# Kernel tuning notes

Measured on AMD Instinct MI355X. Metric: run time of the kernel, lower is better.

Reference implementation:

```python
import jax, jax.numpy as jnp
import numpy as np

HEADS = 8
DIM_HEAD = 64
NUM_PATHWAYS = 281
SCALE = DIM_HEAD ** -0.5


def setup_inputs() -> dict:
    key = jax.random.key(0)
    k1, k2 = jax.random.split(key)
    b, n, dim = 4, 12281, 512  # n = 281 pathway tokens + 12000 histology patch tokens
    x = jax.random.normal(k1, (b, n, dim), dtype=jnp.float32)
    W_qkv = jax.random.normal(k2, (dim, 3 * HEADS * DIM_HEAD), dtype=jnp.float32) * 0.02
    return {"x": x, "W_qkv": W_qkv}


def reference(x, W_qkv):
    b, n, _ = x.shape
    h, d, m = HEADS, DIM_HEAD, NUM_PATHWAYS
    qkv = x @ W_qkv  # [b, n, 3*h*d]
    q, k, v = jnp.split(qkv, 3, axis=-1)
    # [b, n, h*d] -> [b, h, n, d]
    to_bhnd = lambda t: t.reshape(b, n, h, d).transpose(0, 2, 1, 3)
    q, k, v = to_bhnd(q), to_bhnd(k), to_bhnd(v)
    q = q * SCALE

    q_path, q_hist = q[:, :, :m], q[:, :, m:]
    k_path, k_hist = k[:, :, :m], k[:, :, m:]
    v_path, v_hist = v[:, :, :m], v[:, :, m:]

    # histology queries attend to pathway keys: [b, h, n_hist, m]
    attn_hist = jax.nn.softmax(jnp.einsum('bhid,bhjd->bhij', q_hist, k_path), axis=-1)
    # pathway queries attend to histology keys: [b, h, m, n_hist]
    attn_path = jax.nn.softmax(jnp.einsum('bhid,bhjd->bhij', q_path, k_hist), axis=-1)

    out_pathways = jnp.einsum('bhij,bhjd->bhid', attn_hist, v_path)   # [b, h, n_hist, d]
    out_histology = jnp.einsum('bhij,bhjd->bhid', attn_path, v_hist)  # [b, h, m, d]

    cross_token = jnp.concatenate([out_pathways, out_histology], axis=2)  # [b, h, n, d]
    return cross_token.transpose(0, 2, 1, 3).reshape(b, n, h * d)
```

## Files before the change

### kernel.cpp

```cpp
#include <hip/hip_runtime.h>
#include <hip/hip_bf16.h>

#define BATCH  4
#define NTOK   12281
#define DIMIN  512
#define HEADS  8
#define DHEAD  64
#define MPATH  281
#define NHIST  12000
#define QKVC   1536
#define QSCALE 0.180336884f
#define ROWS   (BATCH * NTOK)
#define MPAD   49152
#define NSPLIT 16
#define KSPL   768
#define PROWS  320
#define HROWS  12032
#define M1B    640
#define M0B    1504
#define QPAD   4096

typedef __attribute__((ext_vector_type(8)))  short        short8v;
typedef __attribute__((ext_vector_type(4)))  float        f32x4;
typedef __attribute__((ext_vector_type(16))) float        f32x16;
typedef __attribute__((ext_vector_type(4)))  unsigned int uint4v;

__device__ __forceinline__ unsigned short f2bf(float f) {
    unsigned x = __builtin_bit_cast(unsigned, f);
    return (unsigned short)((x + 0x7fffu + ((x >> 16) & 1u)) >> 16);
}
__device__ __forceinline__ unsigned pk2(float a, float b) {
    return (unsigned)f2bf(a) | ((unsigned)f2bf(b) << 16);
}
__device__ __forceinline__ unsigned pk2n(float a, float b) {
    unsigned r;
    asm("v_cvt_pk_bf16_f32 %0, %1, %2" : "=v"(r) : "v"(a), "v"(b));
    return r;
}
__device__ __forceinline__ void plswap(unsigned &a, unsigned &b) {
    asm("v_permlane32_swap_b32 %0, %1" : "+v"(a), "+v"(b));
}
__device__ __forceinline__ float fexp2(float x) {
    return __builtin_amdgcn_exp2f(x);
}
__device__ __forceinline__ short8v ld8(const unsigned short* p) {
    return *reinterpret_cast<const short8v*>(p);
}
__device__ __forceinline__ f32x16 MFMA32(short8v a, short8v b, f32x16 c) {
    return __builtin_amdgcn_mfma_f32_32x32x16_bf16(a, b, c, 0, 0, 0);
}
__device__ __forceinline__ void gl16(const char* g, char* l) {
    __builtin_amdgcn_global_load_lds(
        (const __attribute__((address_space(1))) unsigned int*)g,
        (__attribute__((address_space(3))) unsigned int*)l, 16, 0, 0);
}

__global__ __launch_bounds__(256)
void convert_x(const float* __restrict__ x, unsigned short* __restrict__ xb)
{
    size_t i = ((size_t)blockIdx.x * 256 + threadIdx.x) * 8;
    if (i >= (size_t)MPAD * DIMIN) return;
    uint4v o;
    if (i < (size_t)ROWS * DIMIN) {
        float4 a = *reinterpret_cast<const float4*>(x + i);
        float4 b = *reinterpret_cast<const float4*>(x + i + 4);
        o[0] = pk2(a.x, a.y); o[1] = pk2(a.z, a.w);
        o[2] = pk2(b.x, b.y); o[3] = pk2(b.z, b.w);
    } else {
        o[0] = o[1] = o[2] = o[3] = 0u;
    }
    *reinterpret_cast<uint4v*>(xb + i) = o;
}

__global__ __launch_bounds__(256)
void wt_convert(const float* __restrict__ w, unsigned short* __restrict__ wt)
{
    __shared__ unsigned short Ls[64][72];
    const int k0 = blockIdx.x * 64;
    const int n0 = blockIdx.y * 64;
    const int t  = threadIdx.x;
    const int lr = t >> 2;
    const int c0 = (t & 3) * 16;

    const float* sp = w + (size_t)(k0 + lr) * QKVC + n0 + c0;
    #pragma unroll
    for (int j = 0; j < 16; j += 4) {
        float4 a = *reinterpret_cast<const float4*>(sp + j);
        Ls[lr][c0 + j + 0] = f2bf(a.x);
        Ls[lr][c0 + j + 1] = f2bf(a.y);
        Ls[lr][c0 + j + 2] = f2bf(a.z);
        Ls[lr][c0 + j + 3] = f2bf(a.w);
    }
    __syncthreads();

    alignas(16) unsigned short tmp[16];
    #pragma unroll
    for (int j = 0; j < 16; ++j) tmp[j] = Ls[c0 + j][lr];
    unsigned short* dp = wt + (size_t)(n0 + lr) * DIMIN + k0 + c0;
    *reinterpret_cast<short8v*>(dp)     = *reinterpret_cast<short8v*>(&tmp[0]);
    *reinterpret_cast<short8v*>(dp + 8) = *reinterpret_cast<short8v*>(&tmp[8]);
}

__global__ __launch_bounds__(256)
void pad_fill(unsigned short* kpth, unsigned short* vpth,
              unsigned short* khst, unsigned short* vhst)
{
    int i = blockIdx.x * 256 + threadIdx.x;
    const int PPAD = (PROWS - MPATH) * DHEAD;
    const int HPAD = (HROWS - NHIST) * DHEAD;
    if (i < 32 * PPAD) {
        int bh = i / PPAD, r = i - bh * PPAD;
        size_t off = ((size_t)bh * PROWS + MPATH) * DHEAD + r;
        kpth[off] = 0; vpth[off] = 0;
    }
    if (i < 32 * HPAD) {
        int bh = i / HPAD, r = i - bh * HPAD;
        size_t off = ((size_t)bh * HROWS + NHIST) * DHEAD + r;
        khst[off] = 0; vhst[off] = 0;
    }
}

__global__ __launch_bounds__(256, 2)
void qkv_mfma(const unsigned short* __restrict__ xb, const unsigned short* __restrict__ wt,
              unsigned short* __restrict__ qb,
              unsigned short* __restrict__ kpth, unsigned short* __restrict__ khst,
              unsigned short* __restrict__ vpth, unsigned short* __restrict__ vhst)
{
    __shared__ char lds[65536];
    const int tid  = threadIdx.x;
    const int lane = tid & 63;
    const int wid  = tid >> 6;
    const int wr   = wid >> 1;
    const int wc   = wid & 1;

    int id  = blockIdx.x;
    int wg  = (id & 7) * 576 + (id >> 3);
    const int mt = wg / 12, nt = wg - mt * 12;
    const int bm = mt * 128, bn = nt * 128;

    const int arow0 = tid >> 3;
    const int acolS = ((tid & 7) << 4) ^ ((arow0 & 7) << 4);
    const char* xsrc = (const char*)xb + (((size_t)(bm + arow0)) << 10) + acolS;
    const char* wsrc = (const char*)wt + (((size_t)(bn + arow0)) << 10) + acolS;
    char* ldsA = lds + wid * 1024;
    char* ldsB = lds + 16384 + wid * 1024;

    const int rA   = wr * 64 + (lane & 15);
    const int rB   = wc * 64 + (lane & 15);
    const int hi16 = (lane >> 4) << 4;
    const int sxA  = (rA & 7) << 4;
    const int sxB  = (rB & 7) << 4;

    f32x4 acc[4][4];
    #pragma unroll
    for (int m = 0; m < 4; ++m)
        #pragma unroll
        for (int n = 0; n < 4; ++n)
            #pragma unroll
            for (int r = 0; r < 4; ++r) acc[m][n][r] = 0.f;

    auto STAGE = [&](int bufofs, int ks) {
        const char* xs = xsrc + (size_t)ks * 128;
        const char* ws = wsrc + (size_t)ks * 128;
        #pragma unroll
        for (int i = 0; i < 4; ++i)
            gl16(xs + ((size_t)i << 15), ldsA + bufofs + i * 4096);
        #pragma unroll
        for (int i = 0; i < 4; ++i)
            gl16(ws + ((size_t)i << 15), ldsB + bufofs + i * 4096);
    };

    STAGE(0, 0);
    asm volatile("s_waitcnt vmcnt(0)" ::: "memory");
    __syncthreads();

    for (int ks = 0; ks < 8; ++ks) {
        const int cur = ks & 1;
        if (ks < 7) STAGE((cur ^ 1) * 32768, ks + 1);

        const char* A = lds + cur * 32768;
        const char* B = A + 16384;
        #pragma unroll
        for (int kk = 0; kk < 2; ++kk) {
            short8v a[4], b[4];
            #pragma unroll
            for (int m = 0; m < 4; ++m)
                a[m] = *reinterpret_cast<const short8v*>(
                    A + (rA + m * 16) * 128 + ((kk * 64 + hi16) ^ sxA));
            #pragma unroll
            for (int n = 0; n < 4; ++n)
                b[n] = *reinterpret_cast<const short8v*>(
                    B + (rB + n * 16) * 128 + ((kk * 64 + hi16) ^ sxB));
            #pragma unroll
            for (int m = 0; m < 4; ++m)
                #pragma unroll
                for (int n = 0; n < 4; ++n)
                    acc[m][n] = __builtin_amdgcn_mfma_f32_16x16x32_bf16(
                        a[m], b[n], acc[m][n], 0, 0, 0);
        }
        asm volatile("s_waitcnt vmcnt(0)" ::: "memory");
        __syncthreads();
    }

    unsigned short* cl = reinterpret_cast<unsigned short*>(lds);
    const int crow0 = (lane >> 4) * 4;
    const int ccol  = lane & 15;
    #pragma unroll
    for (int n = 0; n < 4; ++n) {
        const int gcb = bn + wc * 64 + n * 16;
        const float scl = (gcb < 512) ? QSCALE : 1.f;
        #pragma unroll
        for (int m = 0; m < 4; ++m) {
            #pragma unroll
            for (int r = 0; r < 4; ++r) {
                int row = wr * 64 + m * 16 + crow0 + r;
                int col = wc * 64 + n * 16 + ccol;
                cl[row * 136 + col] = f2bf(acc[m][n][r] * scl);
            }
        }
    }
    __syncthreads();

    #pragma unroll
    for (int i = 0; i < 8; ++i) {
        const int chunk = tid + i * 256;
        const int row = chunk >> 4;
        const int c8  = (chunk & 15) * 8;
        const int grow = bm + row;
        if (grow < ROWS) {
            uint4v val = *reinterpret_cast<const uint4v*>(cl + row * 136 + c8);
            const int gcol  = bn + c8;
            const int which = gcol >> 9;
            const int rem   = gcol & 511;
            const int hh = rem >> 6, dd = rem & 63;
            const int bb = grow / NTOK;
            const int nn = grow - bb * NTOK;
            const int bh = bb * HEADS + hh;
            unsigned short* dst;
            if (which == 0) {
                dst = qb + ((size_t)bh * NTOK + nn) * DHEAD + dd;
            } else if (which == 1) {
                dst = (nn < MPATH) ? kpth + ((size_t)bh * PROWS + nn) * DHEAD + dd
                                   : khst + ((size_t)bh * HROWS + (nn - MPATH)) * DHEAD + dd;
            } else {
                dst = (nn < MPATH) ? vpth + ((size_t)bh * PROWS + nn) * DHEAD + dd
                                   : vhst + ((size_t)bh * HROWS + (nn - MPATH)) * DHEAD + dd;
            }
            *reinterpret_cast<uint4v*>(dst) = val;
        }
    }
}

__global__ __launch_bounds__(256)
void transpose64(const unsigned short* __restrict__ src, unsigned short* __restrict__ dst,
                 int nrpad)
{
    __shared__ unsigned short Ls[64][72];
    const int bh = blockIdx.y;
    const int r0 = blockIdx.x * 64;
    const unsigned short* s = src + (size_t)bh * nrpad * DHEAD;
    unsigned short*       d = dst + (size_t)bh * nrpad * DHEAD;

    const int t  = threadIdx.x;
    const int lr = t >> 2;
    const int c0 = (t & 3) * 16;

    const unsigned short* sp = s + (size_t)(r0 + lr) * DHEAD + c0;
    *reinterpret_cast<short8v*>(&Ls[lr][c0])     = *reinterpret_cast<const short8v*>(sp);
    *reinterpret_cast<short8v*>(&Ls[lr][c0 + 8]) = *reinterpret_cast<const short8v*>(sp + 8);
    __syncthreads();

    alignas(16) unsigned short tmp[16];
    #pragma unroll
    for (int j = 0; j < 16; ++j) tmp[j] = Ls[c0 + j][lr];
    const int T  = (r0 + c0) >> 5;
    const int kk = (r0 + c0) & 31;
    unsigned short* dp = d + (((size_t)T * 64 + lr) << 5) + kk;
    *reinterpret_cast<short8v*>(dp)     = *reinterpret_cast<short8v*>(&tmp[0]);
    *reinterpret_cast<short8v*>(dp + 8) = *reinterpret_cast<short8v*>(&tmp[8]);
}

#define ATTN_BODY(VC0,VC1,VC2,VC3,VN0,VN1,VN2,VN3,TT)                      \
  do {                                                                     \
    __builtin_amdgcn_s_setprio(1);                                         \
    f32x16 sA = MFMA32(kf0, qA0, SZ);                                      \
    sA = MFMA32(kf1, qA1, sA);                                             \
    sA = MFMA32(kf2, qA2, sA);                                             \
    sA = MFMA32(kf3, qA3, sA);                                             \
    f32x16 sB = MFMA32(kf0, qB0, SZ);                                      \
    sB = MFMA32(kf1, qB1, sB);                                             \
    sB = MFMA32(kf2, qB2, sB);                                             \
    sB = MFMA32(kf3, qB3, sB);                                             \
    __builtin_amdgcn_s_setprio(0);                                         \
    if ((TT) + 1 < ntiles) {               \
      const unsigned short* kn = kr + (size_t)((TT) + 1) * 2048;           \
      kf0 = ld8(kn);      kf1 = ld8(kn + 16);                              \
      kf2 = ld8(kn + 32); kf3 = ld8(kn + 48);                              \
      const unsigned short* vn = vb + (size_t)((TT) + 1) * 2048;           \
      VN0 = ld8(vn);        VN1 = ld8(vn + 16);                            \
      VN2 = ld8(vn + 1024); VN3 = ld8(vn + 1040);                          \
    }                                                                      \
    float psA = 0.f, psB = 0.f;                                            \
    if (mode0 && (TT) == 8) {                   \
      _Pragma("unroll")                                                    \
      for (int r = 0; r < 16; ++r) {                                       \
        int krow = (r & 3) + 8 * (r >> 2) + 4 * hi;                        \
        float eA = (256 + krow >= MPATH) ? 0.f : fexp2(sA[r]);             \
        float eB = (256 + krow >= MPATH) ? 0.f : fexp2(sB[r]);             \
        sA[r] = eA; psA += eA;                                             \
        sB[r] = eB; psB += eB;                                             \
      }                                                                    \
    } else {                                                               \
      _Pragma("unroll")                                                    \
      for (int r = 0; r < 16; ++r) {                                       \
        float eA = fexp2(sA[r]); sA[r] = eA; psA += eA;                    \
        float eB = fexp2(sB[r]); sB[r] = eB; psB += eB;                    \
      }                                                                    \
    }                                                                      \
    lA += psA; lB += psB;                                                  \
    unsigned A0 = pk2n(sA[0],  sA[1]),  A1 = pk2n(sA[2],  sA[3]);          \
    unsigned A2 = pk2n(sA[4],  sA[5]),  A3 = pk2n(sA[6],  sA[7]);          \
    unsigned A4 = pk2n(sA[8],  sA[9]),  A5 = pk2n(sA[10], sA[11]);         \
    unsigned A6 = pk2n(sA[12], sA[13]), A7 = pk2n(sA[14], sA[15]);         \
    plswap(A0, A2); plswap(A1, A3); plswap(A4, A6); plswap(A5, A7);        \
    uint4v wA0, wA1;                                                       \
    wA0[0] = A0; wA0[1] = A1; wA0[2] = A2; wA0[3] = A3;                    \
    wA1[0] = A4; wA1[1] = A5; wA1[2] = A6; wA1[3] = A7;                    \
    short8v paA0 = __builtin_bit_cast(short8v, wA0);                       \
    short8v paA1 = __builtin_bit_cast(short8v, wA1);                       \
    unsigned B0 = pk2n(sB[0],  sB[1]),  B1 = pk2n(sB[2],  sB[3]);          \
    unsigned B2 = pk2n(sB[4],  sB[5]),  B3 = pk2n(sB[6],  sB[7]);          \
    unsigned B4 = pk2n(sB[8],  sB[9]),  B5 = pk2n(sB[10], sB[11]);         \
    unsigned B6 = pk2n(sB[12], sB[13]), B7 = pk2n(sB[14], sB[15]);         \
    plswap(B0, B2); plswap(B1, B3); plswap(B4, B6); plswap(B5, B7);        \
    uint4v wB0, wB1;                                                       \
    wB0[0] = B0; wB0[1] = B1; wB0[2] = B2; wB0[3] = B3;                    \
    wB1[0] = B4; wB1[1] = B5; wB1[2] = B6; wB1[3] = B7;                    \
    short8v paB0 = __builtin_bit_cast(short8v, wB0);                       \
    short8v paB1 = __builtin_bit_cast(short8v, wB1);                       \
    __builtin_amdgcn_s_setprio(1);                                         \
    o0 = MFMA32(paA0, VC0, o0);                                            \
    o0 = MFMA32(paA1, VC1, o0);                                            \
    o1 = MFMA32(paA0, VC2, o1);                                            \
    o1 = MFMA32(paA1, VC3, o1);                                            \
    o2 = MFMA32(paB0, VC0, o2);                                            \
    o2 = MFMA32(paB1, VC1, o2);                                            \
    o3 = MFMA32(paB0, VC2, o3);                                            \
    o3 = MFMA32(paB1, VC3, o3);                                            \
    __builtin_amdgcn_s_setprio(0);                                         \
  } while (0)

__global__ __launch_bounds__(256, 2)
void fused_attn(const unsigned short* __restrict__ qbuf,
                const unsigned short* __restrict__ kpth, const unsigned short* __restrict__ khst,
                const unsigned short* __restrict__ vtp,  const unsigned short* __restrict__ vth,
                float* __restrict__ out,
                float* __restrict__ pl, float* __restrict__ po)
{
    const int wave = threadIdx.x >> 6;
    const int lane = threadIdx.x & 63;
    const int hi   = lane >> 5;
    const int ql   = lane & 31;

    int bh, pw, sp = 0;
    bool mode0;
    if (blockIdx.x < M1B) {
        mode0 = false;
        const int xcd = blockIdx.x & 7;
        const int j   = blockIdx.x >> 3;
        const int w   = j * 4 + wave;
        const int spi = w / 160;
        const int rem = w - spi * 160;
        bh = rem / 5;
        pw = rem - bh * 5;
        sp = xcd + 8 * spi;
    } else {
        mode0 = true;
        const int b0  = blockIdx.x - M1B;
        const int xcd = b0 & 7;
        const int i   = b0 >> 3;
        const int g   = i / 47;
        bh = xcd + 8 * g;
        pw = (i - g * 47) * 4 + wave;
    }

    const int q0 = mode0 ? (MPATH + pw * 64) : (pw * 64);
    const unsigned short* qra = qbuf + ((size_t)bh * NTOK + (q0 + ql)) * DHEAD + hi * 8;
    const unsigned short* qrb = qra + (size_t)32 * DHEAD;
    short8v qA0 = ld8(qra),      qA1 = ld8(qra + 16);
    short8v qA2 = ld8(qra + 32), qA3 = ld8(qra + 48);
    short8v qB0 = ld8(qrb),      qB1 = ld8(qrb + 16);
    short8v qB2 = ld8(qrb + 32), qB3 = ld8(qrb + 48);

    const unsigned short* kr;
    const unsigned short* vb;
    int ntiles;
    if (mode0) {
        kr = kpth + (size_t)bh * PROWS * DHEAD + ql * DHEAD + hi * 8;
        vb = vtp  + (size_t)bh * PROWS * DHEAD + ql * 32 + hi * 8;
        ntiles = 9;
    } else {
        kr = khst + ((size_t)bh * HROWS + (size_t)sp * KSPL) * DHEAD + ql * DHEAD + hi * 8;
        vb = vth  + (size_t)bh * HROWS * DHEAD + (size_t)sp * 24 * 2048 + ql * 32 + hi * 8;
        ntiles = (sp == NSPLIT - 1) ? 15 : 24;
    }

    f32x16 o0, o1, o2, o3, SZ;
    #pragma unroll
    for (int r = 0; r < 16; ++r) { o0[r] = 0.f; o1[r] = 0.f; o2[r] = 0.f; o3[r] = 0.f; SZ[r] = 0.f; }
    float lA = 0.f, lB = 0.f;

    short8v kf0 = ld8(kr), kf1 = ld8(kr + 16), kf2 = ld8(kr + 32), kf3 = ld8(kr + 48);
    short8v va0 = ld8(vb),        va1 = ld8(vb + 16);
    short8v va2 = ld8(vb + 1024), va3 = ld8(vb + 1040);
    short8v vb0 = va0, vb1 = va1, vb2 = va2, vb3 = va3;

    for (int t = 0;;) {
        ATTN_BODY(va0, va1, va2, va3, vb0, vb1, vb2, vb3, t);
        if (++t >= ntiles) break;
        ATTN_BODY(vb0, vb1, vb2, vb3, va0, va1, va2, va3, t);
        if (++t >= ntiles) break;
    }

    const float lAr = lA + __shfl_xor(lA, 32);
    const float lBr = lB + __shfl_xor(lB, 32);

    if (mode0) {
        const int bb = bh >> 3, hh = bh & 7;
        const float liA = 1.0f / lAr;
        const float liB = 1.0f / lBr;
        #pragma unroll
        for (int r = 0; r < 16; ++r) {
            const int row = (r & 3) + 8 * (r >> 2) + 4 * hi;
            {
                float invr = __shfl(liA, row);
                float* op = out + ((size_t)bb * NTOK + (pw * 64 + row)) * (HEADS * DHEAD) + hh * DHEAD;
                op[ql]      = o0[r] * invr;
                op[32 + ql] = o1[r] * invr;
            }
            const int tokB = pw * 64 + 32 + row;
            if (tokB < NHIST) {
                float invr = __shfl(liB, row);
                float* op = out + ((size_t)bb * NTOK + tokB) * (HEADS * DHEAD) + hh * DHEAD;
                op[ql]      = o2[r] * invr;
                op[32 + ql] = o3[r] * invr;
            }
        }
    } else {
        const size_t pbase = ((size_t)bh * NSPLIT + sp) * MPATH;
        if (hi == 0) {
            if (q0 + ql < MPATH)      pl[pbase + q0 + ql]      = lAr;
            if (q0 + 32 + ql < MPATH) pl[pbase + q0 + 32 + ql] = lBr;
        }
        #pragma unroll
        for (int r = 0; r < 16; ++r) {
            const int row = (r & 3) + 8 * (r >> 2) + 4 * hi;
            const int qqA = q0 + row;
            if (qqA < MPATH) {
                float* pp = po + (pbase + qqA) * DHEAD;
                pp[ql]      = o0[r];
                pp[32 + ql] = o1[r];
            }
            const int qqB = q0 + 32 + row;
            if (qqB < MPATH) {
                float* pp = po + (pbase + qqB) * DHEAD;
                pp[ql]      = o2[r];
                pp[32 + ql] = o3[r];
            }
        }
    }
}

__global__ __launch_bounds__(256)
void combine_kernel(const float* __restrict__ pl, const float* __restrict__ po,
                    float* __restrict__ out)
{
    const int idx = blockIdx.x * 256 + threadIdx.x;
    const int dd  = idx & 63;
    const int r   = idx >> 6;
    if (r >= BATCH * HEADS * MPATH) return;
    const int bh = r / MPATH;
    const int jq = r - bh * MPATH;

    const size_t pbase = ((size_t)bh * NSPLIT) * MPATH + jq;
    float L = 0.f, acc = 0.f;
    #pragma unroll
    for (int s = 0; s < NSPLIT; ++s) {
        L   += pl[pbase + (size_t)s * MPATH];
        acc += po[(pbase + (size_t)s * MPATH) * DHEAD + dd];
    }
    const int bb = bh >> 3, hh = bh & 7;
    out[((size_t)bb * NTOK + (NHIST + jq)) * (HEADS * DHEAD) + hh * DHEAD + dd] = acc / L;
}

extern "C" void kernel_launch(void* const* d_in, const int* in_sizes, int n_in,
                              void* d_out, int out_size, void* d_ws, size_t ws_size,
                              hipStream_t stream)
{
    (void)in_sizes; (void)n_in; (void)out_size; (void)ws_size;
    const float* x = (const float*)d_in[0];
    const float* w = (const float*)d_in[1];
    float* out = (float*)d_out;

    const size_t QEL = (size_t)32 * NTOK * DHEAD + QPAD;
    const size_t PEL = (size_t)32 * PROWS * DHEAD;
    const size_t HEL = (size_t)32 * HROWS * DHEAD;

    unsigned short* qb   = (unsigned short*)d_ws;
    unsigned short* kpth = qb   + QEL;
    unsigned short* khst = kpth + PEL;
    unsigned short* vpth = khst + HEL;
    unsigned short* vhst = vpth + PEL;
    unsigned short* vtp  = vhst + HEL;
    unsigned short* vth  = vtp  + PEL;
    unsigned short* xb   = vth  + HEL;
    unsigned short* wtb  = xb   + (size_t)MPAD * DIMIN;
    float* pl = (float*)(wtb + (size_t)QKVC * DIMIN);
    float* po = pl + (size_t)32 * NSPLIT * MPATH;

    convert_x<<<(MPAD * DIMIN / 8 + 255) / 256, 256, 0, stream>>>(x, xb);
    wt_convert<<<dim3(DIMIN / 64, QKVC / 64), 256, 0, stream>>>(w, wtb);
    pad_fill<<<312, 256, 0, stream>>>(kpth, vpth, khst, vhst);

    qkv_mfma<<<(MPAD / 128) * (QKVC / 128), 256, 0, stream>>>(xb, wtb, qb,
                                                              kpth, khst, vpth, vhst);

    transpose64<<<dim3(PROWS / 64, 32), 256, 0, stream>>>(vpth, vtp, PROWS);
    transpose64<<<dim3(HROWS / 64, 32), 256, 0, stream>>>(vhst, vth, HROWS);

    fused_attn<<<M1B + M0B, 256, 0, stream>>>(qb, kpth, khst, vtp, vth, out, pl, po);

    const int rows = BATCH * HEADS * MPATH;
    combine_kernel<<<(rows * DHEAD + 255) / 256, 256, 0, stream>>>(pl, po, out);
}
```

Measured before the change: 282.2 us.

## Merge prep kernels into one launch and compute softmax row sums via MFMA

The three preprocessing kernels (x conversion, weight transpose/convert, pad zeroing) are merged into one launch that dispatches on block index, removing two kernel launches and their gaps. In the attention kernel, the per-tile scalar accumulation of exponentiated scores is replaced by extra MFMAs against a vector of bf16 ones, which yields row sums already laid out per output row. This removes the cross-lane shuffles and scalar adds, at the cost of four extra MFMAs per tile, two more 16-register accumulators, and sums computed from bf16-rounded probabilities, which changes precision slightly. The final division now uses a raw hardware reciprocal instruction.

```diff
diff --git a/kernel.cpp b/kernel.cpp
--- a/kernel.cpp
+++ b/kernel.cpp
@@ -19,6 +19,9 @@
 #define M1B    640
 #define M0B    1504
 #define QPAD   4096
+#define NB_CONV 12288
+#define NB_WT   192
+#define NB_PAD  312
 
 typedef __attribute__((ext_vector_type(8)))  short        short8v;
 typedef __attribute__((ext_vector_type(4)))  float        f32x4;
@@ -43,6 +46,11 @@
 __device__ __forceinline__ float fexp2(float x) {
     return __builtin_amdgcn_exp2f(x);
 }
+__device__ __forceinline__ float frcp(float x) {
+    float r;
+    asm("v_rcp_f32 %0, %1" : "=v"(r) : "v"(x));
+    return r;
+}
 __device__ __forceinline__ short8v ld8(const unsigned short* p) {
     return *reinterpret_cast<const short8v*>(p);
 }
@@ -56,67 +64,65 @@
 }
 
 __global__ __launch_bounds__(256)
-void convert_x(const float* __restrict__ x, unsigned short* __restrict__ xb)
-{
-    size_t i = ((size_t)blockIdx.x * 256 + threadIdx.x) * 8;
-    if (i >= (size_t)MPAD * DIMIN) return;
-    uint4v o;
-    if (i < (size_t)ROWS * DIMIN) {
-        float4 a = *reinterpret_cast<const float4*>(x + i);
-        float4 b = *reinterpret_cast<const float4*>(x + i + 4);
-        o[0] = pk2(a.x, a.y); o[1] = pk2(a.z, a.w);
-        o[2] = pk2(b.x, b.y); o[3] = pk2(b.z, b.w);
-    } else {
-        o[0] = o[1] = o[2] = o[3] = 0u;
-    }
-    *reinterpret_cast<uint4v*>(xb + i) = o;
-}
-
-__global__ __launch_bounds__(256)
-void wt_convert(const float* __restrict__ w, unsigned short* __restrict__ wt)
+void prep_all(const float* __restrict__ x, unsigned short* __restrict__ xb,
+              const float* __restrict__ w, unsigned short* __restrict__ wt,
+              unsigned short* kpth, unsigned short* vpth,
+              unsigned short* khst, unsigned short* vhst)
 {
     __shared__ unsigned short Ls[64][72];
-    const int k0 = blockIdx.x * 64;
-    const int n0 = blockIdx.y * 64;
-    const int t  = threadIdx.x;
-    const int lr = t >> 2;
-    const int c0 = (t & 3) * 16;
-
-    const float* sp = w + (size_t)(k0 + lr) * QKVC + n0 + c0;
-    #pragma unroll
-    for (int j = 0; j < 16; j += 4) {
-        float4 a = *reinterpret_cast<const float4*>(sp + j);
-        Ls[lr][c0 + j + 0] = f2bf(a.x);
-        Ls[lr][c0 + j + 1] = f2bf(a.y);
-        Ls[lr][c0 + j + 2] = f2bf(a.z);
-        Ls[lr][c0 + j + 3] = f2bf(a.w);
-    }
-    __syncthreads();
-
-    alignas(16) unsigned short tmp[16];
-    #pragma unroll
-    for (int j = 0; j < 16; ++j) tmp[j] = Ls[c0 + j][lr];
-    unsigned short* dp = wt + (size_t)(n0 + lr) * DIMIN + k0 + c0;
-    *reinterpret_cast<short8v*>(dp)     = *reinterpret_cast<short8v*>(&tmp[0]);
-    *reinterpret_cast<short8v*>(dp + 8) = *reinterpret_cast<short8v*>(&tmp[8]);
-}
-
-__global__ __launch_bounds__(256)
-void pad_fill(unsigned short* kpth, unsigned short* vpth,
-              unsigned short* khst, unsigned short* vhst)
-{
-    int i = blockIdx.x * 256 + threadIdx.x;
-    const int PPAD = (PROWS - MPATH) * DHEAD;
-    const int HPAD = (HROWS - NHIST) * DHEAD;
-    if (i < 32 * PPAD) {
-        int bh = i / PPAD, r = i - bh * PPAD;
-        size_t off = ((size_t)bh * PROWS + MPATH) * DHEAD + r;
-        kpth[off] = 0; vpth[off] = 0;
-    }
-    if (i < 32 * HPAD) {
-        int bh = i / HPAD, r = i - bh * HPAD;
-        size_t off = ((size_t)bh * HROWS + NHIST) * DHEAD + r;
-        khst[off] = 0; vhst[off] = 0;
+    const int b   = blockIdx.x;
+    const int tid = threadIdx.x;
+
+    if (b < NB_CONV) {
+        size_t i = ((size_t)b * 256 + tid) * 8;
+        uint4v o;
+        if (i < (size_t)ROWS * DIMIN) {
+            float4 a = *reinterpret_cast<const float4*>(x + i);
+            float4 c = *reinterpret_cast<const float4*>(x + i + 4);
+            o[0] = pk2(a.x, a.y); o[1] = pk2(a.z, a.w);
+            o[2] = pk2(c.x, c.y); o[3] = pk2(c.z, c.w);
+        } else {
+            o[0] = o[1] = o[2] = o[3] = 0u;
+        }
+        *reinterpret_cast<uint4v*>(xb + i) = o;
+    } else if (b < NB_CONV + NB_WT) {
+        const int bb = b - NB_CONV;
+        const int k0 = (bb & 7) * 64;
+        const int n0 = (bb >> 3) * 64;
+        const int lr = tid >> 2;
+        const int c0 = (tid & 3) * 16;
+
+        const float* sp = w + (size_t)(k0 + lr) * QKVC + n0 + c0;
+        #pragma unroll
+        for (int j = 0; j < 16; j += 4) {
+            float4 a = *reinterpret_cast<const float4*>(sp + j);
+            Ls[lr][c0 + j + 0] = f2bf(a.x);
+            Ls[lr][c0 + j + 1] = f2bf(a.y);
+            Ls[lr][c0 + j + 2] = f2bf(a.z);
+            Ls[lr][c0 + j + 3] = f2bf(a.w);
+        }
+        __syncthreads();
+
+        alignas(16) unsigned short tmp[16];
+        #pragma unroll
+        for (int j = 0; j < 16; ++j) tmp[j] = Ls[c0 + j][lr];
+        unsigned short* dp = wt + (size_t)(n0 + lr) * DIMIN + k0 + c0;
+        *reinterpret_cast<short8v*>(dp)     = *reinterpret_cast<short8v*>(&tmp[0]);
+        *reinterpret_cast<short8v*>(dp + 8) = *reinterpret_cast<short8v*>(&tmp[8]);
+    } else {
+        const int i = (b - NB_CONV - NB_WT) * 256 + tid;
+        const int PPAD = (PROWS - MPATH) * DHEAD;
+        const int HPAD = (HROWS - NHIST) * DHEAD;
+        if (i < 32 * PPAD) {
+            int bh = i / PPAD, r = i - bh * PPAD;
+            size_t off = ((size_t)bh * PROWS + MPATH) * DHEAD + r;
+            kpth[off] = 0; vpth[off] = 0;
+        }
+        if (i < 32 * HPAD) {
+            int bh = i / HPAD, r = i - bh * HPAD;
+            size_t off = ((size_t)bh * HROWS + NHIST) * DHEAD + r;
+            khst[off] = 0; vhst[off] = 0;
+        }
     }
 }
 
@@ -300,24 +306,20 @@
       VN0 = ld8(vn);        VN1 = ld8(vn + 16);                            \
       VN2 = ld8(vn + 1024); VN3 = ld8(vn + 1040);                          \
     }                                                                      \
-    float psA = 0.f, psB = 0.f;                                            \
     if (mode0 && (TT) == 8) {                   \
       _Pragma("unroll")                                                    \
       for (int r = 0; r < 16; ++r) {                                       \
         int krow = (r & 3) + 8 * (r >> 2) + 4 * hi;                        \
-        float eA = (256 + krow >= MPATH) ? 0.f : fexp2(sA[r]);             \
-        float eB = (256 + krow >= MPATH) ? 0.f : fexp2(sB[r]);             \
-        sA[r] = eA; psA += eA;                                             \
-        sB[r] = eB; psB += eB;                                             \
+        sA[r] = (256 + krow >= MPATH) ? 0.f : fexp2(sA[r]);                \
+        sB[r] = (256 + krow >= MPATH) ? 0.f : fexp2(sB[r]);                \
       }                                                                    \
     } else {                                                               \
       _Pragma("unroll")                                                    \
       for (int r = 0; r < 16; ++r) {                                       \
-        float eA = fexp2(sA[r]); sA[r] = eA; psA += eA;                    \
-        float eB = fexp2(sB[r]); sB[r] = eB; psB += eB;                    \
+        sA[r] = fexp2(sA[r]);                                              \
+        sB[r] = fexp2(sB[r]);                                              \
       }                                                                    \
     }                                                                      \
-    lA += psA; lB += psB;                                                  \
     unsigned A0 = pk2n(sA[0],  sA[1]),  A1 = pk2n(sA[2],  sA[3]);          \
     unsigned A2 = pk2n(sA[4],  sA[5]),  A3 = pk2n(sA[6],  sA[7]);          \
     unsigned A4 = pk2n(sA[8],  sA[9]),  A5 = pk2n(sA[10], sA[11]);         \
@@ -347,6 +349,10 @@
     o2 = MFMA32(paB1, VC1, o2);                                            \
     o3 = MFMA32(paB0, VC2, o3);                                            \
     o3 = MFMA32(paB1, VC3, o3);                                            \
+    olA = MFMA32(paA0, ones8, olA);                                        \
+    olA = MFMA32(paA1, ones8, olA);                                        \
+    olB = MFMA32(paB0, ones8, olB);                                        \
+    olB = MFMA32(paB1, ones8, olB);                                        \
     __builtin_amdgcn_s_setprio(0);                                         \
   } while (0)
 
@@ -405,10 +411,15 @@
         ntiles = (sp == NSPLIT - 1) ? 15 : 24;
     }
 
-    f32x16 o0, o1, o2, o3, SZ;
+    const uint4v onesu = {0x3F803F80u, 0x3F803F80u, 0x3F803F80u, 0x3F803F80u};
+    const short8v ones8 = __builtin_bit_cast(short8v, onesu);
+
+    f32x16 o0, o1, o2, o3, olA, olB, SZ;
     #pragma unroll
-    for (int r = 0; r < 16; ++r) { o0[r] = 0.f; o1[r] = 0.f; o2[r] = 0.f; o3[r] = 0.f; SZ[r] = 0.f; }
-    float lA = 0.f, lB = 0.f;
+    for (int r = 0; r < 16; ++r) {
+        o0[r] = 0.f; o1[r] = 0.f; o2[r] = 0.f; o3[r] = 0.f;
+        olA[r] = 0.f; olB[r] = 0.f; SZ[r] = 0.f;
+    }
 
     short8v kf0 = ld8(kr), kf1 = ld8(kr + 16), kf2 = ld8(kr + 32), kf3 = ld8(kr + 48);
     short8v va0 = ld8(vb),        va1 = ld8(vb + 16);
@@ -422,25 +433,20 @@
         if (++t >= ntiles) break;
     }
 
-    const float lAr = lA + __shfl_xor(lA, 32);
-    const float lBr = lB + __shfl_xor(lB, 32);
-
     if (mode0) {
         const int bb = bh >> 3, hh = bh & 7;
-        const float liA = 1.0f / lAr;
-        const float liB = 1.0f / lBr;
         #pragma unroll
         for (int r = 0; r < 16; ++r) {
             const int row = (r & 3) + 8 * (r >> 2) + 4 * hi;
             {
-                float invr = __shfl(liA, row);
+                const float invr = frcp(olA[r]);
                 float* op = out + ((size_t)bb * NTOK + (pw * 64 + row)) * (HEADS * DHEAD) + hh * DHEAD;
                 op[ql]      = o0[r] * invr;
                 op[32 + ql] = o1[r] * invr;
             }
             const int tokB = pw * 64 + 32 + row;
             if (tokB < NHIST) {
-                float invr = __shfl(liB, row);
+                const float invr = frcp(olB[r]);
                 float* op = out + ((size_t)bb * NTOK + tokB) * (HEADS * DHEAD) + hh * DHEAD;
                 op[ql]      = o2[r] * invr;
                 op[32 + ql] = o3[r] * invr;
@@ -448,9 +454,13 @@
         }
     } else {
         const size_t pbase = ((size_t)bh * NSPLIT + sp) * MPATH;
-        if (hi == 0) {
-            if (q0 + ql < MPATH)      pl[pbase + q0 + ql]      = lAr;
-            if (q0 + 32 + ql < MPATH) pl[pbase + q0 + 32 + ql] = lBr;
+        if (ql == 0) {
+            #pragma unroll
+            for (int r = 0; r < 16; ++r) {
+                const int row = (r & 3) + 8 * (r >> 2) + 4 * hi;
+                if (q0 + row < MPATH)      pl[pbase + q0 + row]      = olA[r];
+                if (q0 + 32 + row < MPATH) pl[pbase + q0 + 32 + row] = olB[r];
+            }
         }
         #pragma unroll
         for (int r = 0; r < 16; ++r) {
@@ -518,9 +528,8 @@
     float* pl = (float*)(wtb + (size_t)QKVC * DIMIN);
     float* po = pl + (size_t)32 * NSPLIT * MPATH;
 
-    convert_x<<<(MPAD * DIMIN / 8 + 255) / 256, 256, 0, stream>>>(x, xb);
-    wt_convert<<<dim3(DIMIN / 64, QKVC / 64), 256, 0, stream>>>(w, wtb);
-    pad_fill<<<312, 256, 0, stream>>>(kpth, vpth, khst, vhst);
+    prep_all<<<NB_CONV + NB_WT + NB_PAD, 256, 0, stream>>>(x, xb, w, wtb,
+                                                           kpth, vpth, khst, vhst);
 
     qkv_mfma<<<(MPAD / 128) * (QKVC / 128), 256, 0, stream>>>(xb, wtb, qb,
                                                               kpth, khst, vpth, vhst);
```

New measurement: 331.0 us. +17.3%, slower.
